# Kernel optimization log

Hardware: AMD Instinct MI355X
Metric: run time of the kernel (lower is better)

Reference implementation:

```python
import jax, jax.numpy as jnp
import numpy as np

N_NODES = 65536
N_GRID = 32768
N_EDGES = 524288
HID = 128
EDGE_FEAT = 6


def _linear_params(key, fan_in, fan_out):
    k1, k2 = jax.random.split(key)
    bound = 1.0 / np.sqrt(fan_in)
    w = jax.random.uniform(k1, (fan_in, fan_out), jnp.float32, -bound, bound)
    b = jax.random.uniform(k2, (fan_out,), jnp.float32, -bound, bound)
    return w, b


def setup_inputs() -> dict:
    key = jax.random.key(0)
    ks = jax.random.split(key, 10)
    node_embedding = jax.random.normal(ks[0], (N_NODES, HID), jnp.float32)
    node_pos = jax.random.normal(ks[1], (N_NODES, 3), jnp.float32)
    grid_pos = jax.random.normal(ks[2], (N_GRID, 3), jnp.float32)
    # index_i: random source nodes; index_j: destination grid cells, arranged so
    # every grid cell receives >= 1 message (bincount mean is well-defined).
    index_i = jax.random.randint(ks[3], (N_EDGES,), 0, N_NODES, jnp.int64)
    index_j = jax.random.permutation(ks[4], jnp.arange(N_EDGES, dtype=jnp.int64) % N_GRID)
    edge_index = jnp.stack([index_i, index_j], axis=0)
    ew1, eb1 = _linear_params(ks[5], EDGE_FEAT, HID)
    ew2, eb2 = _linear_params(ks[6], HID, HID)
    mw1, mb1 = _linear_params(ks[7], 2 * HID, HID)
    mw2, mb2 = _linear_params(ks[8], HID, HID)
    uw1, ub1 = _linear_params(ks[9], HID, HID)
    uw2, ub2 = _linear_params(jax.random.fold_in(key, 99), HID, HID)
    return {
        "node_embedding": node_embedding, "node_pos": node_pos,
        "grid_pos": grid_pos, "edge_index": edge_index,
        "ew1": ew1, "eb1": eb1, "ew2": ew2, "eb2": eb2,
        "mw1": mw1, "mb1": mb1, "mw2": mw2, "mb2": mb2,
        "uw1": uw1, "ub1": ub1, "uw2": uw2, "ub2": ub2,
    }


def reference(node_embedding, node_pos, grid_pos, edge_index,
              ew1, eb1, ew2, eb2, mw1, mb1, mw2, mb2, uw1, ub1, uw2, ub2):
    index_i, index_j = edge_index[0], edge_index[1]
    n_grid = grid_pos.shape[0]
    # message: gather positions, edge MLP, concat with gathered node embedding, message MLP
    edge_attr = jnp.concatenate([node_pos[index_i], grid_pos[index_j]], axis=-1)  # [E, 6]
    pos_emb = jax.nn.silu(edge_attr @ ew1 + eb1) @ ew2 + eb2                      # [E, H]
    msg_in = jnp.concatenate([node_embedding[index_i], pos_emb], axis=-1)        # [E, 2H]
    message = jax.nn.silu(msg_in @ mw1 + mb1) @ mw2 + mb2                        # [E, H]
    # update: segment mean over destination grid index, then update MLP
    sums = jax.ops.segment_sum(message, index_j, num_segments=n_grid)            # [G, H]
    counts = jax.ops.segment_sum(jnp.ones((message.shape[0],), message.dtype),
                                 index_j, num_segments=n_grid)                    # [G]
    mean = sums / counts[:, None]
    update = jax.nn.silu(mean @ uw1 + ub1) @ uw2 + ub2                           # [G, H]
    return update
```

## Files before the change

kernel.cpp:

```cpp
#include <hip/hip_runtime.h>
#include <hip/hip_bf16.h>

#define HID 128
#define LDK 136
#define CPB 4
#define CAP 16

#define WT_M1L 0
#define WT_T   16384
#define WT_W2U 32768
#define WT_U2  49152
#define WT_TOTAL 65536

typedef __attribute__((ext_vector_type(8))) short bf16x8;
typedef __attribute__((ext_vector_type(4))) float f32x4;

#define MFMA(a, b, c) __builtin_amdgcn_mfma_f32_16x16x32_bf16(a, b, c, 0, 0, 0)

__device__ __forceinline__ float silu_f(float x) {
    return x * (1.0f / (1.0f + __expf(-x)));
}

__device__ __forceinline__ short f2b(float x) {
    __hip_bfloat16 h = __float2bfloat16(x);
    return *(short*)&h;
}

__device__ __forceinline__ float b2f(unsigned short u) {
    union { unsigned u32; float f; } v;
    v.u32 = ((unsigned)u) << 16;
    return v.f;
}

template<int LDB>
__device__ __forceinline__ void gemm128(f32x4 acc[4][2], const short* actb,
                                        const short* __restrict__ w0)
{
    const short* __restrict__ w1 = w0 + 16 * LDB;
    #pragma unroll
    for (int ks = 0; ks < 4; ++ks) {
        bf16x8 wa = *(const bf16x8*)(w0 + ks * 32);
        bf16x8 wb = *(const bf16x8*)(w1 + ks * 32);
        #pragma unroll
        for (int e4 = 0; e4 < 4; ++e4) {
            bf16x8 a = *(const bf16x8*)(actb + e4 * (16 * LDK) + ks * 32);
            acc[e4][0] = MFMA(a, wa, acc[e4][0]);
            acc[e4][1] = MFMA(a, wb, acc[e4][1]);
        }
    }
}

extern "C" __global__ void __launch_bounds__(256)
prep0(const int* __restrict__ ei, int* __restrict__ cnt, int* __restrict__ bin, int E,
      const float* __restrict__ ew1, const float* __restrict__ eb1,
      const float* __restrict__ ew2, const float* __restrict__ eb2,
      const float* __restrict__ mw1, const float* __restrict__ mw2,
      const float* __restrict__ mb2,
      const float* __restrict__ uw1, const float* __restrict__ ub1,
      const float* __restrict__ uw2,
      const float* __restrict__ gpos,
      short* __restrict__ wt, float* __restrict__ bias2, float* __restrict__ bU,
      float* __restrict__ preC, int G)
{
    int nbin = (E + 255) / 256;
    int b = blockIdx.x;
    int t = threadIdx.x;
    if (b < nbin) {
        int e = b * 256 + t;
        if (e < E) {
            int j = ei[E + e];
            int i = ei[e];
            int slot = atomicAdd(&cnt[j], 1);
            if (slot < CAP) bin[(size_t)j * CAP + slot] = i;
        }
        return;
    }
    b -= nbin;
    if (b < 128) {
        int idx = b * 256 + t;
        if (idx < 16384) {
            int n = idx >> 7, k = idx & 127;
            wt[WT_M1L + idx] = f2b(mw1[k * HID + n]);
        } else {
            int r = idx - 16384;
            int n = r >> 7, k = r & 127;
            wt[WT_U2 + r] = f2b(uw2[k * HID + n]);
        }
        return;
    }
    b -= 128;
    if (b < 64) {
        int idx = b * 256 + t;
        int n = idx >> 7, a = idx & 127;
        const float* er = ew2 + (size_t)a * HID;
        float s = 0.0f;
        for (int f = 0; f < HID; ++f)
            s = fmaf(er[f], mw1[(size_t)(HID + f) * HID + n], s);
        wt[WT_T + idx] = f2b(s);
        return;
    }
    b -= 64;
    if (b < 64) {
        int idx = b * 256 + t;
        int n = idx >> 7, a = idx & 127;
        const float* mr = mw2 + (size_t)a * HID;
        float s = 0.0f;
        for (int f = 0; f < HID; ++f)
            s = fmaf(mr[f], uw1[(size_t)f * HID + n], s);
        wt[WT_W2U + idx] = f2b(s);
        return;
    }
    b -= 64;
    if (b < 1) {
        if (t < HID) {
            float s = 0.0f;
            for (int f = 0; f < HID; ++f)
                s = fmaf(eb2[f], mw1[(size_t)(HID + f) * HID + t], s);
            bias2[t] = s;
        } else if (t < 2 * HID) {
            int n = t - HID;
            float s = 0.0f;
            for (int f = 0; f < HID; ++f)
                s = fmaf(mb2[f], uw1[(size_t)f * HID + n], s);
            bU[n] = s + ub1[n];
        }
        return;
    }
    b -= 1;
    {
        int idx = b * 256 + t;
        if (idx < G * 16) {
            int cell = idx >> 4, f0 = (idx & 15) * 8;
            const float* gp = gpos + (size_t)cell * 3;
            float g0 = gp[0], g1 = gp[1], g2 = gp[2];
            const float* w3 = ew1 + 3 * HID + f0;
            const float* w4 = ew1 + 4 * HID + f0;
            const float* w5 = ew1 + 5 * HID + f0;
            const float* bb = eb1 + f0;
            float o[8];
            #pragma unroll
            for (int j = 0; j < 8; ++j)
                o[j] = g0 * w3[j] + g1 * w4[j] + g2 * w5[j] + bb[j];
            float* dst = preC + (size_t)cell * HID + f0;
            *(float4*)dst       = make_float4(o[0], o[1], o[2], o[3]);
            *(float4*)(dst + 4) = make_float4(o[4], o[5], o[6], o[7]);
        }
    }
}

extern "C" __global__ void __launch_bounds__(256, 4)
prep_gemm(const float* __restrict__ emb, const float* __restrict__ mb1,
          const float* __restrict__ bias2, const short* __restrict__ wt,
          unsigned short* __restrict__ pre)
{
    __shared__ short s_x[64 * LDK];
    const int t  = threadIdx.x;
    const int r0 = blockIdx.x * 64;

    {
        int row = t >> 2, part = t & 3;
        const float4* src = (const float4*)(emb + (size_t)(r0 + row) * HID + part * 32);
        short* dst = s_x + row * LDK + part * 32;
        #pragma unroll
        for (int c = 0; c < 4; ++c) {
            float4 v0 = src[c * 2], v1 = src[c * 2 + 1];
            short4 a4, b4;
            a4.x = f2b(v0.x); a4.y = f2b(v0.y); a4.z = f2b(v0.z); a4.w = f2b(v0.w);
            b4.x = f2b(v1.x); b4.y = f2b(v1.y); b4.z = f2b(v1.z); b4.w = f2b(v1.w);
            *(short4*)(dst + c * 8)     = a4;
            *(short4*)(dst + c * 8 + 4) = b4;
        }
    }
    __syncthreads();

    const int lane = t & 63, q = lane & 15, h = lane >> 4, nb = (t >> 6) * 32;
    f32x4 acc[4][2];
    #pragma unroll
    for (int m = 0; m < 4; ++m) { acc[m][0] = (f32x4)(0.0f); acc[m][1] = (f32x4)(0.0f); }
    gemm128<128>(acc, s_x + q * LDK + h * 8, wt + WT_M1L + (nb + q) * 128 + h * 8);

    #pragma unroll
    for (int nf = 0; nf < 2; ++nf) {
        int n = nb + nf * 16 + q;
        float bb = mb1[n] + bias2[n];
        #pragma unroll
        for (int m = 0; m < 4; ++m)
            #pragma unroll
            for (int r = 0; r < 4; ++r)
                pre[(size_t)(r0 + m * 16 + h * 4 + r) * HID + n] =
                    f2b(acc[m][nf][r] + bb);
    }
}

extern "C" __global__ void __launch_bounds__(256, 6)
edge_kernel(const float* __restrict__ npos,
            const float* __restrict__ ew1,
            const short* __restrict__ wt,
            const int* __restrict__ bin,
            const unsigned short* __restrict__ pre,
            const float* __restrict__ preC,
            unsigned short* __restrict__ gsum)
{
    __shared__ short s_h1[64 * LDK];
    __shared__ short s_red[4 * HID];
    __shared__ int   s_bin[64];

    const int t  = threadIdx.x;
    const int c0 = blockIdx.x * CPB;
    const int lane = t & 63, q = lane & 15, h = lane >> 4, nb = (t >> 6) * 32;

    if (t < 64) s_bin[t] = bin[c0 * CAP + t];

    int idL[4];
    #pragma unroll
    for (int e4 = 0; e4 < 4; ++e4)
        idL[e4] = bin[c0 * CAP + e4 * 16 + q];

    float np0[4], np1[4], np2[4];
    #pragma unroll
    for (int e4 = 0; e4 < 4; ++e4) {
        const float* p = npos + (size_t)idL[e4] * 3;
        np0[e4] = p[0]; np1[e4] = p[1]; np2[e4] = p[2];
    }

    const int f00 = nb + h * 4;
    short* wx = s_h1 + q * LDK + nb + h * 4;

    #pragma unroll
    for (int nf = 0; nf < 2; ++nf) {
        int f0 = f00 + nf * 16;
        float4 wn0 = *(const float4*)(ew1 + 0 * HID + f0);
        float4 wn1 = *(const float4*)(ew1 + 1 * HID + f0);
        float4 wn2 = *(const float4*)(ew1 + 2 * HID + f0);
        #pragma unroll
        for (int e4 = 0; e4 < 4; ++e4) {
            float4 pc = *(const float4*)(preC + (size_t)(c0 + e4) * HID + f0);
            float z0 = silu_f(pc.x + np0[e4] * wn0.x + np1[e4] * wn1.x + np2[e4] * wn2.x);
            float z1 = silu_f(pc.y + np0[e4] * wn0.y + np1[e4] * wn1.y + np2[e4] * wn2.y);
            float z2 = silu_f(pc.z + np0[e4] * wn0.z + np1[e4] * wn1.z + np2[e4] * wn2.z);
            float z3 = silu_f(pc.w + np0[e4] * wn0.w + np1[e4] * wn1.w + np2[e4] * wn2.w);
            short4 s4;
            s4.x = f2b(z0); s4.y = f2b(z1); s4.z = f2b(z2); s4.w = f2b(z3);
            *(short4*)(wx + e4 * (16 * LDK) + nf * 16) = s4;
        }
    }
    __syncthreads();

    unsigned short pA[4][4], pB[4][4];
    #pragma unroll
    for (int m = 0; m < 4; ++m) {
        #pragma unroll
        for (int r = 0; r < 4; ++r) {
            int id = s_bin[m * 16 + h * 4 + r];
            const unsigned short* pr = pre + (size_t)id * HID;
            pA[m][r] = pr[nb + q];
            pB[m][r] = pr[nb + 16 + q];
        }
    }

    f32x4 acc[4][2];
    #pragma unroll
    for (int m = 0; m < 4; ++m) { acc[m][0] = (f32x4)(0.0f); acc[m][1] = (f32x4)(0.0f); }
    gemm128<128>(acc, s_h1 + q * LDK + h * 8, wt + WT_T + (nb + q) * 128 + h * 8);

    #pragma unroll
    for (int m = 0; m < 4; ++m) {
        #pragma unroll
        for (int nf = 0; nf < 2; ++nf) {
            f32x4 v = acc[m][nf];
            float s = silu_f(v[0] + b2f(nf ? pB[m][0] : pA[m][0]));
            s += silu_f(v[1] + b2f(nf ? pB[m][1] : pA[m][1]));
            s += silu_f(v[2] + b2f(nf ? pB[m][2] : pA[m][2]));
            s += silu_f(v[3] + b2f(nf ? pB[m][3] : pA[m][3]));
            s += __shfl_xor(s, 16);
            s += __shfl_xor(s, 32);
            if (h == 0)
                s_red[m * HID + nb + nf * 16 + q] = f2b(s);
        }
    }
    __syncthreads();

    {
        const unsigned* src = (const unsigned*)s_red;
        unsigned* dst = (unsigned*)(gsum + (size_t)c0 * HID);
        dst[t] = src[t];
    }
}

extern "C" __global__ void __launch_bounds__(256, 4)
update_kernel(const float* __restrict__ ub2, const float* __restrict__ bU,
              const short* __restrict__ wt, const int* __restrict__ cnt,
              const unsigned short* __restrict__ gsum, float* __restrict__ out)
{
    __shared__ short s_x[64 * LDK];
    __shared__ short s_u[64 * LDK];
    __shared__ float s_inv[64];

    const int t  = threadIdx.x;
    const int c0 = blockIdx.x * 64;

    {
        int row = t >> 2, part = t & 3;
        const uint4* src = (const uint4*)(gsum + (size_t)(c0 + row) * HID + part * 32);
        uint4* dst = (uint4*)(s_x + row * LDK + part * 32);
        dst[0] = src[0]; dst[1] = src[1]; dst[2] = src[2]; dst[3] = src[3];
    }
    if (t < 64) {
        int c = cnt[c0 + t];
        s_inv[t] = 1.0f / (float)(c > 0 ? c : 1);
    }
    __syncthreads();

    const int lane = t & 63, q = lane & 15, h = lane >> 4, nb = (t >> 6) * 32;
    f32x4 acc[4][2];
    #pragma unroll
    for (int m = 0; m < 4; ++m) { acc[m][0] = (f32x4)(0.0f); acc[m][1] = (f32x4)(0.0f); }
    gemm128<128>(acc, s_x + q * LDK + h * 8, wt + WT_W2U + (nb + q) * 128 + h * 8);

    #pragma unroll
    for (int nf = 0; nf < 2; ++nf) {
        int n = nb + nf * 16 + q;
        float bb = bU[n];
        #pragma unroll
        for (int m = 0; m < 4; ++m) {
            #pragma unroll
            for (int r = 0; r < 4; ++r) {
                int row = m * 16 + h * 4 + r;
                s_u[row * LDK + n] = f2b(silu_f(acc[m][nf][r] * s_inv[row] + bb));
            }
        }
    }
    __syncthreads();

    #pragma unroll
    for (int m = 0; m < 4; ++m) { acc[m][0] = (f32x4)(0.0f); acc[m][1] = (f32x4)(0.0f); }
    gemm128<128>(acc, s_u + q * LDK + h * 8, wt + WT_U2 + (nb + q) * 128 + h * 8);

    #pragma unroll
    for (int nf = 0; nf < 2; ++nf) {
        int n = nb + nf * 16 + q;
        float bb = ub2[n];
        #pragma unroll
        for (int m = 0; m < 4; ++m)
            #pragma unroll
            for (int r = 0; r < 4; ++r)
                out[(size_t)(c0 + m * 16 + h * 4 + r) * HID + n] = acc[m][nf][r] + bb;
    }
}

extern "C" void kernel_launch(void* const* d_in, const int* in_sizes, int n_in,
                              void* d_out, int out_size, void* d_ws, size_t ws_size,
                              hipStream_t stream)
{
    const float* emb  = (const float*)d_in[0];
    const float* npos = (const float*)d_in[1];
    const float* gpos = (const float*)d_in[2];
    const int*   ei   = (const int*)d_in[3];
    const float* ew1  = (const float*)d_in[4];
    const float* eb1  = (const float*)d_in[5];
    const float* ew2  = (const float*)d_in[6];
    const float* eb2  = (const float*)d_in[7];
    const float* mw1  = (const float*)d_in[8];
    const float* mb1  = (const float*)d_in[9];
    const float* mw2  = (const float*)d_in[10];
    const float* mb2  = (const float*)d_in[11];
    const float* uw1  = (const float*)d_in[12];
    const float* ub1  = (const float*)d_in[13];
    const float* uw2  = (const float*)d_in[14];
    const float* ub2  = (const float*)d_in[15];

    const int E  = in_sizes[3] / 2;
    const int G  = in_sizes[2] / 3;
    const int NN = in_sizes[0] / HID;

    unsigned short* pre  = (unsigned short*)d_ws;
    float*          preC = (float*)(pre + (size_t)NN * HID);
    unsigned short* gsum = (unsigned short*)(preC + (size_t)G * HID);
    char* p = (char*)(gsum + (size_t)G * HID);
    int*   cnt = (int*)p;                 p += (size_t)G * 4;
    int*   bin = (int*)p;                 p += (size_t)G * CAP * 4;
    short* wt  = (short*)p;               p += (size_t)WT_TOTAL * 2;
    float* bias2 = (float*)p;             p += HID * 4;
    float* bU    = (float*)p;

    hipMemsetAsync(cnt, 0, (size_t)G * 4, stream);

    int nbin  = (E + 255) / 256;
    int nprec = (G * 16 + 255) / 256;
    prep0<<<nbin + 128 + 64 + 64 + 1 + nprec, 256, 0, stream>>>(
        ei, cnt, bin, E, ew1, eb1, ew2, eb2, mw1, mw2, mb2, uw1, ub1, uw2,
        gpos, wt, bias2, bU, preC, G);
    prep_gemm<<<NN / 64, 256, 0, stream>>>(emb, mb1, bias2, wt, pre);
    edge_kernel<<<G / CPB, 256, 0, stream>>>(npos, ew1, wt, bin, pre, preC, gsum);
    update_kernel<<<G / 64, 256, 0, stream>>>(ub2, bU, wt, cnt, gsum, (float*)d_out);
}
```

Baseline: 155.8 us.

## Assign one cell per wavefront in edge kernel, building MFMA A-fragments in registers

The edge kernel now gives each wavefront one grid cell with its 16 edges and all 128 output features. The first-layer SiLU activations are built straight into MFMA A-operand registers instead of being staged through a shared-memory tile, which removes the LDS tile and one block barrier. Each wave now reads the full 128x128 weight matrix from global/L2 rather than a 32-column slice, so per-wave weight traffic and register pressure go up. The launch bound drops from 6 to 4 blocks to make room for the larger accumulator set.

```diff
diff --git a/kernel.cpp b/kernel.cpp
--- a/kernel.cpp
+++ b/kernel.cpp
@@ -192,7 +192,7 @@
     }
 }
 
-extern "C" __global__ void __launch_bounds__(256, 6)
+extern "C" __global__ void __launch_bounds__(256, 4)
 edge_kernel(const float* __restrict__ npos,
             const float* __restrict__ ew1,
             const short* __restrict__ wt,
@@ -201,82 +201,79 @@
             const float* __restrict__ preC,
             unsigned short* __restrict__ gsum)
 {
-    __shared__ short s_h1[64 * LDK];
-    __shared__ short s_red[4 * HID];
-    __shared__ int   s_bin[64];
+    __shared__ short s_red[CPB * HID];
 
     const int t  = threadIdx.x;
     const int c0 = blockIdx.x * CPB;
-    const int lane = t & 63, q = lane & 15, h = lane >> 4, nb = (t >> 6) * 32;
-
-    if (t < 64) s_bin[t] = bin[c0 * CAP + t];
-
-    int idL[4];
-    #pragma unroll
-    for (int e4 = 0; e4 < 4; ++e4)
-        idL[e4] = bin[c0 * CAP + e4 * 16 + q];
-
-    float np0[4], np1[4], np2[4];
-    #pragma unroll
-    for (int e4 = 0; e4 < 4; ++e4) {
-        const float* p = npos + (size_t)idL[e4] * 3;
-        np0[e4] = p[0]; np1[e4] = p[1]; np2[e4] = p[2];
-    }
-
-    const int f00 = nb + h * 4;
-    short* wx = s_h1 + q * LDK + nb + h * 4;
-
-    #pragma unroll
-    for (int nf = 0; nf < 2; ++nf) {
-        int f0 = f00 + nf * 16;
-        float4 wn0 = *(const float4*)(ew1 + 0 * HID + f0);
-        float4 wn1 = *(const float4*)(ew1 + 1 * HID + f0);
-        float4 wn2 = *(const float4*)(ew1 + 2 * HID + f0);
-        #pragma unroll
-        for (int e4 = 0; e4 < 4; ++e4) {
-            float4 pc = *(const float4*)(preC + (size_t)(c0 + e4) * HID + f0);
-            float z0 = silu_f(pc.x + np0[e4] * wn0.x + np1[e4] * wn1.x + np2[e4] * wn2.x);
-            float z1 = silu_f(pc.y + np0[e4] * wn0.y + np1[e4] * wn1.y + np2[e4] * wn2.y);
-            float z2 = silu_f(pc.z + np0[e4] * wn0.z + np1[e4] * wn1.z + np2[e4] * wn2.z);
-            float z3 = silu_f(pc.w + np0[e4] * wn0.w + np1[e4] * wn1.w + np2[e4] * wn2.w);
-            short4 s4;
-            s4.x = f2b(z0); s4.y = f2b(z1); s4.z = f2b(z2); s4.w = f2b(z3);
-            *(short4*)(wx + e4 * (16 * LDK) + nf * 16) = s4;
-        }
-    }
-    __syncthreads();
-
-    unsigned short pA[4][4], pB[4][4];
-    #pragma unroll
-    for (int m = 0; m < 4; ++m) {
-        #pragma unroll
-        for (int r = 0; r < 4; ++r) {
-            int id = s_bin[m * 16 + h * 4 + r];
-            const unsigned short* pr = pre + (size_t)id * HID;
-            pA[m][r] = pr[nb + q];
-            pB[m][r] = pr[nb + 16 + q];
-        }
-    }
-
-    f32x4 acc[4][2];
-    #pragma unroll
-    for (int m = 0; m < 4; ++m) { acc[m][0] = (f32x4)(0.0f); acc[m][1] = (f32x4)(0.0f); }
-    gemm128<128>(acc, s_h1 + q * LDK + h * 8, wt + WT_T + (nb + q) * 128 + h * 8);
-
-    #pragma unroll
-    for (int m = 0; m < 4; ++m) {
-        #pragma unroll
-        for (int nf = 0; nf < 2; ++nf) {
-            f32x4 v = acc[m][nf];
-            float s = silu_f(v[0] + b2f(nf ? pB[m][0] : pA[m][0]));
-            s += silu_f(v[1] + b2f(nf ? pB[m][1] : pA[m][1]));
-            s += silu_f(v[2] + b2f(nf ? pB[m][2] : pA[m][2]));
-            s += silu_f(v[3] + b2f(nf ? pB[m][3] : pA[m][3]));
-            s += __shfl_xor(s, 16);
-            s += __shfl_xor(s, 32);
-            if (h == 0)
-                s_red[m * HID + nb + nf * 16 + q] = f2b(s);
-        }
+    const int lane = t & 63, q = lane & 15, h = lane >> 4;
+    const int w = t >> 6;
+    const int cell = c0 + w;
+
+    int myid = bin[(size_t)cell * CAP + q];
+    const float* np = npos + (size_t)myid * 3;
+    float n0 = np[0], n1 = np[1], n2 = np[2];
+
+    bf16x8 afrag[4];
+    #pragma unroll
+    for (int ks = 0; ks < 4; ++ks) {
+        int k0 = ks * 32 + h * 8;
+        float4 wa0 = *(const float4*)(ew1 + 0 * HID + k0);
+        float4 wa1 = *(const float4*)(ew1 + 0 * HID + k0 + 4);
+        float4 wb0 = *(const float4*)(ew1 + 1 * HID + k0);
+        float4 wb1 = *(const float4*)(ew1 + 1 * HID + k0 + 4);
+        float4 wc0 = *(const float4*)(ew1 + 2 * HID + k0);
+        float4 wc1 = *(const float4*)(ew1 + 2 * HID + k0 + 4);
+        float4 pc0 = *(const float4*)(preC + (size_t)cell * HID + k0);
+        float4 pc1 = *(const float4*)(preC + (size_t)cell * HID + k0 + 4);
+        union { short s[8]; bf16x8 v; } o;
+        o.s[0] = f2b(silu_f(pc0.x + n0 * wa0.x + n1 * wb0.x + n2 * wc0.x));
+        o.s[1] = f2b(silu_f(pc0.y + n0 * wa0.y + n1 * wb0.y + n2 * wc0.y));
+        o.s[2] = f2b(silu_f(pc0.z + n0 * wa0.z + n1 * wb0.z + n2 * wc0.z));
+        o.s[3] = f2b(silu_f(pc0.w + n0 * wa0.w + n1 * wb0.w + n2 * wc0.w));
+        o.s[4] = f2b(silu_f(pc1.x + n0 * wa1.x + n1 * wb1.x + n2 * wc1.x));
+        o.s[5] = f2b(silu_f(pc1.y + n0 * wa1.y + n1 * wb1.y + n2 * wc1.y));
+        o.s[6] = f2b(silu_f(pc1.z + n0 * wa1.z + n1 * wb1.z + n2 * wc1.z));
+        o.s[7] = f2b(silu_f(pc1.w + n0 * wa1.w + n1 * wb1.w + n2 * wc1.w));
+        afrag[ks] = o.v;
+    }
+
+    int ide[4];
+    #pragma unroll
+    for (int r = 0; r < 4; ++r)
+        ide[r] = bin[(size_t)cell * CAP + h * 4 + r];
+    unsigned short pg[4][8];
+    #pragma unroll
+    for (int r = 0; r < 4; ++r) {
+        const unsigned short* pr = pre + (size_t)ide[r] * HID + q;
+        #pragma unroll
+        for (int f = 0; f < 8; ++f)
+            pg[r][f] = pr[f * 16];
+    }
+
+    f32x4 acc[8];
+    #pragma unroll
+    for (int f = 0; f < 8; ++f) acc[f] = (f32x4)(0.0f);
+    const short* wT = wt + WT_T + q * 128 + h * 8;
+    #pragma unroll
+    for (int ks = 0; ks < 4; ++ks) {
+        #pragma unroll
+        for (int f = 0; f < 8; ++f) {
+            bf16x8 b = *(const bf16x8*)(wT + f * (16 * 128) + ks * 32);
+            acc[f] = MFMA(afrag[ks], b, acc[f]);
+        }
+    }
+
+    #pragma unroll
+    for (int f = 0; f < 8; ++f) {
+        f32x4 v = acc[f];
+        float s = silu_f(v[0] + b2f(pg[0][f]));
+        s += silu_f(v[1] + b2f(pg[1][f]));
+        s += silu_f(v[2] + b2f(pg[2][f]));
+        s += silu_f(v[3] + b2f(pg[3][f]));
+        s += __shfl_xor(s, 16);
+        s += __shfl_xor(s, 32);
+        if (h == 0)
+            s_red[w * HID + f * 16 + q] = f2b(s);
     }
     __syncthreads();
 
```

New measurement: 247.3 us. 1.59x slower.
